# Optimization experiments

Hardware: AMD Instinct MI355X
Metric: run time of the kernel (lower is better)

## Reference

```python
import jax, jax.numpy as jnp
import numpy as np

DILS = [2 ** i for i in range(9)] * 7  # 27 residual-only layers + 36 layers with skip
N0 = 27  # first 27 layers (dilations0) do not contribute to skip connections


def _dconv(x, w, b, d):
    # dilated 'same' conv1d: x [B,C,T], w [O,I,3]
    y = jax.lax.conv_general_dilated(x, w, (1,), [(d, d)], rhs_dilation=(d,),
                                     dimension_numbers=('NCH', 'OIH', 'NCH'))
    return y + b[None, :, None]


def _pw(x, w, b):
    # 1x1 conv: w [O,C], x [B,C,T]
    return jnp.einsum('oc,bct->bot', w, x) + b[None, :, None]


def setup_inputs() -> dict:
    key = jax.random.key(0)
    ks = jax.random.split(key, 13)
    B, T, rd, sd, qd, L = 8, 16384, 128, 128, 256, 63
    s = 0.05
    f = lambda k, sh: jax.random.normal(k, sh, jnp.float32) * s
    return {
        'x': jax.random.normal(ks[0], (B, 1, T), jnp.float32),
        'causal_w': f(ks[1], (rd, 1, 25)),
        'causal_b': f(ks[2], (rd,)),
        'dcnn_w': f(ks[3], (L, rd, rd, 3)),
        'dcnn_b': f(ks[4], (L, rd)),
        'dense_w': f(ks[5], (L, rd, rd)),
        'dense_b': f(ks[6], (L, rd)),
        'skip_w': f(ks[7], (L, sd, rd)),
        'skip_b': f(ks[8], (L, sd)),
        'post1_w': f(ks[9], (sd, sd)),
        'post1_b': f(ks[10], (sd,)),
        'post2_w': f(ks[11], (qd, sd)),
        'post2_b': f(ks[12], (qd,)),
    }


def reference(x, causal_w, causal_b, dcnn_w, dcnn_b, dense_w, dense_b,
              skip_w, skip_b, post1_w, post1_b, post2_w, post2_b):
    # causal conv: kernel 25, padding 12 ('same')
    x = jax.lax.conv_general_dilated(x, causal_w, (1,), [(12, 12)],
                                     dimension_numbers=('NCH', 'OIH', 'NCH'))
    x = x + causal_b[None, :, None]
    B, _, T = x.shape
    skip = jnp.zeros((B, skip_w.shape[1], T), x.dtype)
    for cnt, d in enumerate(DILS):
        xin = x
        h = jax.nn.relu(x)
        h = jax.nn.relu(_dconv(h, dcnn_w[cnt], dcnn_b[cnt], d))
        if cnt >= N0:
            skip = skip + _pw(h, skip_w[cnt], skip_b[cnt])
        x = _pw(h, dense_w[cnt], dense_b[cnt]) + xin
    h = jax.nn.relu(_pw(jax.nn.relu(skip), post1_w, post1_b))
    return _pw(h, post2_w, post2_b)
```

## Files before the change

### kernel.cpp

```cpp
#include <hip/hip_runtime.h>

#define RD     128
#define TT     128
#define TLEN   16384
#define NB     8
#define NLAYER 63
#define N0SKIP 27
#define QD     256
#define PADR   136

typedef short bf16x8 __attribute__((ext_vector_type(8)));
typedef float f32x4  __attribute__((ext_vector_type(4)));

__device__ __forceinline__ unsigned short f2bf(float f) {
  unsigned u = __float_as_uint(f);
  u += 0x7fffu + ((u >> 16) & 1u);
  return (unsigned short)(u >> 16);
}
__device__ __forceinline__ short f2bf_relu(float f) {
  f = f > 0.f ? f : 0.f;
  unsigned u = __float_as_uint(f);
  u += 0x7fffu + ((u >> 16) & 1u);
  return (short)(u >> 16);
}

__device__ __forceinline__ void mfma_gemm(const unsigned short* __restrict__ aw,
                                          const short* sx, int rowbase,
                                          int c0w, int t0w, int n, int q,
                                          f32x4 (&acc)[4][4]) {
#pragma unroll
  for (int ks = 0; ks < 4; ++ks) {
    const int i0 = ks * 32 + q * 8;
    bf16x8 a[4], bb[4];
#pragma unroll
    for (int ct = 0; ct < 4; ++ct)
      a[ct] = *(const bf16x8*)&aw[(size_t)(c0w + ct * 16 + n) * RD + i0];
#pragma unroll
    for (int tt = 0; tt < 4; ++tt)
      bb[tt] = *(const bf16x8*)&sx[(rowbase + t0w + tt * 16 + n) * PADR + i0];
#pragma unroll
    for (int ct = 0; ct < 4; ++ct)
#pragma unroll
      for (int tt = 0; tt < 4; ++tt)
        acc[ct][tt] = __builtin_amdgcn_mfma_f32_16x16x32_bf16(a[ct], bb[tt],
                                                              acc[ct][tt], 0, 0, 0);
  }
}

__device__ __forceinline__ void zero_acc(f32x4 (&acc)[4][4]) {
#pragma unroll
  for (int i = 0; i < 4; ++i)
#pragma unroll
    for (int j = 0; j < 4; ++j) acc[i][j] = (f32x4){0.f, 0.f, 0.f, 0.f};
}

__device__ __forceinline__ void stage_rows(short* sx, int rowbase,
                                           const float* __restrict__ xb,
                                           int tstart, int nrows, int tid) {
  for (int idx = tid; idx < nrows * 32; idx += 256) {
    const int r = idx >> 5, c4 = (idx & 31) << 2;
    const int tg = tstart + r;
    float4 v = make_float4(0.f, 0.f, 0.f, 0.f);
    if ((unsigned)tg < (unsigned)TLEN)
      v = *(const float4*)&xb[(size_t)tg * RD + c4];
    short4 o;
    o.x = f2bf_relu(v.x); o.y = f2bf_relu(v.y);
    o.z = f2bf_relu(v.z); o.w = f2bf_relu(v.w);
    *(short4*)&sx[(rowbase + r) * PADR + c4] = o;
  }
}

__device__ __forceinline__ void store_act_bf16(short* dst, const f32x4 (&acc)[4][4],
                                               const float* __restrict__ bias,
                                               int c0w, int t0w, int n, int q) {
#pragma unroll
  for (int ct = 0; ct < 4; ++ct) {
    const int c = c0w + ct * 16 + q * 4;
    const float4 bb = *(const float4*)&bias[c];
#pragma unroll
    for (int tt = 0; tt < 4; ++tt) {
      const int t = t0w + tt * 16 + n;
      const f32x4 A = acc[ct][tt];
      short4 o;
      o.x = f2bf_relu(A[0] + bb.x);
      o.y = f2bf_relu(A[1] + bb.y);
      o.z = f2bf_relu(A[2] + bb.z);
      o.w = f2bf_relu(A[3] + bb.w);
      *(short4*)&dst[t * PADR + c] = o;
    }
  }
}

__device__ __forceinline__ void epi_accum(float* __restrict__ dst,
                                          const float* __restrict__ src,
                                          const float* __restrict__ bias,
                                          const f32x4 (&acc)[4][4],
                                          int c0w, int t0w, int n, int q) {
#pragma unroll
  for (int ct = 0; ct < 4; ++ct) {
    const int c = c0w + ct * 16 + q * 4;
    const float4 bb = *(const float4*)&bias[c];
#pragma unroll
    for (int tt = 0; tt < 4; ++tt) {
      const int t = t0w + tt * 16 + n;
      float4 r = *(const float4*)&src[(size_t)t * RD + c];
      const f32x4 A = acc[ct][tt];
      r.x += A[0] + bb.x; r.y += A[1] + bb.y;
      r.z += A[2] + bb.z; r.w += A[3] + bb.w;
      *(float4*)&dst[(size_t)t * RD + c] = r;
    }
  }
}

__global__ __launch_bounds__(256, 2) void layer_kernel(
    const float* __restrict__ x_in, float* __restrict__ x_out,
    float* __restrict__ skip,
    const unsigned short* __restrict__ wconv,
    const float* __restrict__ bconv,
    const unsigned short* __restrict__ wdense, const float* __restrict__ bdense,
    const unsigned short* __restrict__ wskip,  const float* __restrict__ bskip,
    int dil, int do_skip) {
  __shared__ short sx[256 * PADR];

  const int tid = threadIdx.x;
  const int b   = blockIdx.x >> 7;
  const int t0  = (blockIdx.x & 127) << 7;
  const int lane = tid & 63;
  const int n = lane & 15, q = lane >> 4;
  const int w = tid >> 6;
  const int c0w = (w & 1) * 64, t0w = (w >> 1) * 64;
  const float* xb = x_in + (size_t)b * TLEN * RD;

  f32x4 acc[4][4];
  zero_acc(acc);

  if (dil <= 64) {
    stage_rows(sx, 0, xb, t0 - dil, 128 + 2 * dil, tid);
    __syncthreads();
    for (int k = 0; k < 3; ++k)
      mfma_gemm(wconv + (size_t)k * RD * RD, sx, k * dil, c0w, t0w, n, q, acc);
  } else {
    stage_rows(sx, 0, xb, t0 - dil, 128, tid);
    __syncthreads();
    stage_rows(sx, 128, xb, t0, 128, tid);
    mfma_gemm(wconv, sx, 0, c0w, t0w, n, q, acc);
    __syncthreads();
    stage_rows(sx, 0, xb, t0 + dil, 128, tid);
    mfma_gemm(wconv + (size_t)RD * RD, sx, 128, c0w, t0w, n, q, acc);
    __syncthreads();
    mfma_gemm(wconv + (size_t)2 * RD * RD, sx, 0, c0w, t0w, n, q, acc);
  }
  __syncthreads();

  store_act_bf16(sx, acc, bconv, c0w, t0w, n, q);
  __syncthreads();

  zero_acc(acc);
  mfma_gemm(wdense, sx, 0, c0w, t0w, n, q, acc);
  {
    float* xo = x_out + ((size_t)b * TLEN + t0) * RD;
    const float* xi = x_in + ((size_t)b * TLEN + t0) * RD;
    epi_accum(xo, xi, bdense, acc, c0w, t0w, n, q);
  }

  if (do_skip) {
    zero_acc(acc);
    mfma_gemm(wskip, sx, 0, c0w, t0w, n, q, acc);
    float* sp = skip + ((size_t)b * TLEN + t0) * RD;
    epi_accum(sp, sp, bskip, acc, c0w, t0w, n, q);
  }
}

__global__ __launch_bounds__(256) void causal_kernel(const float* __restrict__ x,
                                                     const float* __restrict__ w,
                                                     const float* __restrict__ bias,
                                                     float* __restrict__ y) {
  __shared__ float xw[152];
  __shared__ float wl[RD * 25];
  __shared__ float bl[RD];
  const int tid = threadIdx.x;
  const int b   = blockIdx.x >> 7;
  const int t0  = (blockIdx.x & 127) << 7;
  for (int i = tid; i < RD * 25; i += 256) wl[i] = w[i];
  if (tid < RD) bl[tid] = bias[tid];
  for (int i = tid; i < 152; i += 256) {
    const int tg = t0 - 12 + i;
    xw[i] = ((unsigned)tg < (unsigned)TLEN) ? x[(size_t)b * TLEN + tg] : 0.f;
  }
  __syncthreads();
  const int c = tid & 127, tp = tid >> 7;
  float* yb = y + ((size_t)b * TLEN + t0) * RD + c;
  const float bc = bl[c];
  for (int i = 0; i < 64; ++i) {
    const int tl = i * 2 + tp;
    float s = bc;
#pragma unroll
    for (int k = 0; k < 25; ++k) s = fmaf(wl[c * 25 + k], xw[tl + k], s);
    yb[(size_t)tl * RD] = s;
  }
}

__global__ __launch_bounds__(256, 1) void post_kernel(
    const float* __restrict__ skip,
    const unsigned short* __restrict__ p1, const float* __restrict__ p1b,
    const unsigned short* __restrict__ p2, const float* __restrict__ p2b,
    float* __restrict__ out) {
  __shared__ short sb[128 * PADR];
  __shared__ short h1[128 * PADR];
  __shared__ float ost[128 * 132];

  const int tid = threadIdx.x;
  const int b   = blockIdx.x >> 7;
  const int t0  = (blockIdx.x & 127) << 7;
  const int lane = tid & 63;
  const int n = lane & 15, q = lane >> 4;
  const int w = tid >> 6;
  const int c0w = (w & 1) * 64, t0w = (w >> 1) * 64;
  const float* skb = skip + ((size_t)b * TLEN + t0) * RD;

  for (int idx = tid; idx < 128 * 32; idx += 256) {
    const int r = idx >> 5, c4 = (idx & 31) << 2;
    float4 v = *(const float4*)&skb[(size_t)r * RD + c4];
    short4 o;
    o.x = f2bf_relu(v.x); o.y = f2bf_relu(v.y);
    o.z = f2bf_relu(v.z); o.w = f2bf_relu(v.w);
    *(short4*)&sb[r * PADR + c4] = o;
  }
  __syncthreads();

  f32x4 acc[4][4];
  zero_acc(acc);
  mfma_gemm(p1, sb, 0, c0w, t0w, n, q, acc);
  store_act_bf16(h1, acc, p1b, c0w, t0w, n, q);
  __syncthreads();

  for (int half = 0; half < 2; ++half) {
    zero_acc(acc);
    mfma_gemm(p2 + (size_t)half * RD * RD, h1, 0, c0w, t0w, n, q, acc);
#pragma unroll
    for (int ct = 0; ct < 4; ++ct) {
      const int c = c0w + ct * 16 + q * 4;
      const float4 bb = *(const float4*)&p2b[half * RD + c];
#pragma unroll
      for (int tt = 0; tt < 4; ++tt) {
        const int t = t0w + tt * 16 + n;
        const f32x4 A = acc[ct][tt];
        ost[(c + 0) * 132 + t] = A[0] + bb.x;
        ost[(c + 1) * 132 + t] = A[1] + bb.y;
        ost[(c + 2) * 132 + t] = A[2] + bb.z;
        ost[(c + 3) * 132 + t] = A[3] + bb.w;
      }
    }
    __syncthreads();
    float* ob = out + ((size_t)b * QD + half * RD) * TLEN + t0;
    for (int idx = tid; idx < 128 * 32; idx += 256) {
      const int r = idx >> 5, t4 = (idx & 31) << 2;
      const float4 v = *(const float4*)&ost[r * 132 + t4];
      *(float4*)&ob[(size_t)r * TLEN + t4] = v;
    }
    __syncthreads();
  }
}

__global__ __launch_bounds__(256) void cvt_kernel(const float* __restrict__ in,
                                                  unsigned short* __restrict__ out,
                                                  int total) {
  const int i = blockIdx.x * 256 + threadIdx.x;
  if (i < total) out[i] = f2bf(in[i]);
}
__global__ __launch_bounds__(256) void cvt_conv_kernel(const float* __restrict__ in,
                                                       unsigned short* __restrict__ out,
                                                       int total) {
  const int idx = blockIdx.x * 256 + threadIdx.x;
  if (idx >= total) return;
  const int ci = idx & 127, co = (idx >> 7) & 127, lk = idx >> 14;
  const int k = lk % 3, l = lk / 3;
  out[idx] = f2bf(in[(((size_t)l * RD + co) * RD + ci) * 3 + k]);
}

extern "C" void kernel_launch(void* const* d_in, const int* in_sizes, int n_in,
                              void* d_out, int out_size, void* d_ws, size_t ws_size,
                              hipStream_t stream) {
  const float* x        = (const float*)d_in[0];
  const float* causal_w = (const float*)d_in[1];
  const float* causal_b = (const float*)d_in[2];
  const float* dcnn_w   = (const float*)d_in[3];
  const float* dcnn_b   = (const float*)d_in[4];
  const float* dense_w  = (const float*)d_in[5];
  const float* dense_b  = (const float*)d_in[6];
  const float* skip_w   = (const float*)d_in[7];
  const float* skip_b   = (const float*)d_in[8];
  const float* post1_w  = (const float*)d_in[9];
  const float* post1_b  = (const float*)d_in[10];
  const float* post2_w  = (const float*)d_in[11];
  const float* post2_b  = (const float*)d_in[12];
  float* out = (float*)d_out;

  const size_t XN = (size_t)NB * TLEN * RD;
  float* ws  = (float*)d_ws;
  float* xA  = ws;
  float* xB  = xA + XN;
  float* skp = xB + XN;
  unsigned short* wc  = (unsigned short*)(skp + XN);
  unsigned short* wd  = wc  + (size_t)NLAYER * 3 * RD * RD;
  unsigned short* wsk = wd  + (size_t)NLAYER * RD * RD;
  unsigned short* p1  = wsk + (size_t)NLAYER * RD * RD;
  unsigned short* p2  = p1  + RD * RD;

  const int tconv = NLAYER * 3 * RD * RD;
  const int t2    = NLAYER * RD * RD;
  cvt_conv_kernel<<<(tconv + 255) / 256, 256, 0, stream>>>(dcnn_w, wc, tconv);
  cvt_kernel<<<(t2 + 255) / 256, 256, 0, stream>>>(dense_w, wd, t2);
  cvt_kernel<<<(t2 + 255) / 256, 256, 0, stream>>>(skip_w, wsk, t2);
  cvt_kernel<<<(RD * RD + 255) / 256, 256, 0, stream>>>(post1_w, p1, RD * RD);
  cvt_kernel<<<(QD * RD + 255) / 256, 256, 0, stream>>>(post2_w, p2, QD * RD);

  causal_kernel<<<NB * (TLEN / TT), 256, 0, stream>>>(x, causal_w, causal_b, xA);
  hipMemsetAsync(skp, 0, XN * sizeof(float), stream);

  const float* src = xA;
  float* dst = xB;
  for (int l = 0; l < NLAYER; ++l) {
    const int dil = 1 << (l % 9);
    layer_kernel<<<NB * (TLEN / TT), 256, 0, stream>>>(
        src, dst, skp,
        wc  + (size_t)l * 3 * RD * RD, dcnn_b  + (size_t)l * RD,
        wd  + (size_t)l * RD * RD,     dense_b + (size_t)l * RD,
        wsk + (size_t)l * RD * RD,     skip_b  + (size_t)l * RD,
        dil, (l >= N0SKIP) ? 1 : 0);
    const float* tmp = src; src = dst; dst = (float*)tmp;
  }

  post_kernel<<<NB * (TLEN / TT), 256, 0, stream>>>(skp, p1, post1_b, p2, post2_b, out);
}
```

Measured before the change: 5.231 ms.

## Store bf16 relu'd activations, defer skip GEMMs into gather kernel with post-processing

Each layer now writes a bf16 copy of relu(x) next to the fp32 residual. The next layer stages bf16 directly into a 192-row circular shared buffer with no conversion, which raises occupancy to 3 blocks per SM. Per-layer skip accumulation (an fp32 read-modify-write of the skip tensor) is replaced by storing the bf16 hidden activations. A gather kernel then runs all skip GEMMs in one register accumulation with double-buffered staging, fused with the post1/post2 layers. This trades extra workspace (up to 36 bf16 activation copies) and extra bf16 writes for less fp32 skip traffic and one fewer kernel.

After: 7.559 ms. 44.5% more time.

```diff
diff --git a/kernel.cpp b/kernel.cpp
--- a/kernel.cpp
+++ b/kernel.cpp
@@ -6,8 +6,10 @@
 #define NB     8
 #define NLAYER 63
 #define N0SKIP 27
+#define NSKIP  36
 #define QD     256
 #define PADR   136
+#define CROWS  192
 
 typedef short bf16x8 __attribute__((ext_vector_type(8)));
 typedef float f32x4  __attribute__((ext_vector_type(4)));
@@ -24,9 +26,25 @@
   return (short)(u >> 16);
 }
 
+__device__ __forceinline__ void zero_acc(f32x4 (&acc)[4][4]) {
+#pragma unroll
+  for (int i = 0; i < 4; ++i)
+#pragma unroll
+    for (int j = 0; j < 4; ++j) acc[i][j] = (f32x4){0.f, 0.f, 0.f, 0.f};
+}
+
+__device__ __forceinline__ void mk_rows(int rows[4], int t0w, int n, int s) {
+#pragma unroll
+  for (int tt = 0; tt < 4; ++tt) {
+    int r = t0w + tt * 16 + n + s;
+    if (r >= CROWS) r -= CROWS;
+    rows[tt] = r;
+  }
+}
+
 __device__ __forceinline__ void mfma_gemm(const unsigned short* __restrict__ aw,
-                                          const short* sx, int rowbase,
-                                          int c0w, int t0w, int n, int q,
+                                          const short* sx, const int rows[4],
+                                          int c0w, int n, int q,
                                           f32x4 (&acc)[4][4]) {
 #pragma unroll
   for (int ks = 0; ks < 4; ++ks) {
@@ -37,7 +55,7 @@
       a[ct] = *(const bf16x8*)&aw[(size_t)(c0w + ct * 16 + n) * RD + i0];
 #pragma unroll
     for (int tt = 0; tt < 4; ++tt)
-      bb[tt] = *(const bf16x8*)&sx[(rowbase + t0w + tt * 16 + n) * PADR + i0];
+      bb[tt] = *(const bf16x8*)&sx[rows[tt] * PADR + i0];
 #pragma unroll
     for (int ct = 0; ct < 4; ++ct)
 #pragma unroll
@@ -47,26 +65,26 @@
   }
 }
 
-__device__ __forceinline__ void zero_acc(f32x4 (&acc)[4][4]) {
-#pragma unroll
-  for (int i = 0; i < 4; ++i)
-#pragma unroll
-    for (int j = 0; j < 4; ++j) acc[i][j] = (f32x4){0.f, 0.f, 0.f, 0.f};
-}
-
-__device__ __forceinline__ void stage_rows(short* sx, int rowbase,
-                                           const float* __restrict__ xb,
-                                           int tstart, int nrows, int tid) {
-  for (int idx = tid; idx < nrows * 32; idx += 256) {
-    const int r = idx >> 5, c4 = (idx & 31) << 2;
+__device__ __forceinline__ void stage_circ(short* sx, const unsigned short* __restrict__ xrb,
+                                           int tstart, int count, int slot0, int tid) {
+  const int tot = count << 4;
+  for (int idx = tid; idx < tot; idx += 256) {
+    const int r = idx >> 4, ck = (idx & 15) << 3;
     const int tg = tstart + r;
-    float4 v = make_float4(0.f, 0.f, 0.f, 0.f);
+    int4 v = {0, 0, 0, 0};
     if ((unsigned)tg < (unsigned)TLEN)
-      v = *(const float4*)&xb[(size_t)tg * RD + c4];
-    short4 o;
-    o.x = f2bf_relu(v.x); o.y = f2bf_relu(v.y);
-    o.z = f2bf_relu(v.z); o.w = f2bf_relu(v.w);
-    *(short4*)&sx[(rowbase + r) * PADR + c4] = o;
+      v = *(const int4*)&xrb[(size_t)tg * RD + ck];
+    int slot = slot0 + r;
+    if (slot >= CROWS) slot -= CROWS;
+    *(int4*)&sx[slot * PADR + ck] = v;
+  }
+}
+
+__device__ __forceinline__ void stage_tile(short* dst, const unsigned short* __restrict__ src,
+                                           int tid) {
+  for (int idx = tid; idx < 128 * 16; idx += 256) {
+    const int r = idx >> 4, ck = (idx & 15) << 3;
+    *(int4*)&dst[r * PADR + ck] = *(const int4*)&src[(size_t)r * RD + ck];
   }
 }
 
@@ -112,15 +130,16 @@
   }
 }
 
-__global__ __launch_bounds__(256, 2) void layer_kernel(
-    const float* __restrict__ x_in, float* __restrict__ x_out,
+__global__ __launch_bounds__(256, 3) void layer_kernel(
+    const unsigned short* __restrict__ xr_in, const float* __restrict__ x_in,
+    float* __restrict__ x_out, unsigned short* __restrict__ xr_out,
+    unsigned short* __restrict__ h_out,
     float* __restrict__ skip,
-    const unsigned short* __restrict__ wconv,
-    const float* __restrict__ bconv,
+    const unsigned short* __restrict__ wconv, const float* __restrict__ bconv,
     const unsigned short* __restrict__ wdense, const float* __restrict__ bdense,
-    const unsigned short* __restrict__ wskip,  const float* __restrict__ bskip,
-    int dil, int do_skip) {
-  __shared__ short sx[256 * PADR];
+    const unsigned short* __restrict__ wskip, const float* __restrict__ bskip,
+    int dil) {
+  __shared__ short sx[CROWS * PADR];
 
   const int tid = threadIdx.x;
   const int b   = blockIdx.x >> 7;
@@ -129,52 +148,196 @@
   const int n = lane & 15, q = lane >> 4;
   const int w = tid >> 6;
   const int c0w = (w & 1) * 64, t0w = (w >> 1) * 64;
-  const float* xb = x_in + (size_t)b * TLEN * RD;
+  const unsigned short* xrb = xr_in + (size_t)b * TLEN * RD;
 
   f32x4 acc[4][4];
   zero_acc(acc);
-
-  if (dil <= 64) {
-    stage_rows(sx, 0, xb, t0 - dil, 128 + 2 * dil, tid);
+  int rows[4];
+
+  if (dil <= 32) {
+    stage_circ(sx, xrb, t0 - dil, 128 + 2 * dil, 0, tid);
     __syncthreads();
-    for (int k = 0; k < 3; ++k)
-      mfma_gemm(wconv + (size_t)k * RD * RD, sx, k * dil, c0w, t0w, n, q, acc);
+#pragma unroll
+    for (int k = 0; k < 3; ++k) {
+      mk_rows(rows, t0w, n, k * dil);
+      mfma_gemm(wconv + (size_t)k * RD * RD, sx, rows, c0w, n, q, acc);
+    }
+  } else if (dil == 64) {
+    stage_circ(sx, xrb, t0 - 64, 192, 0, tid);
+    __syncthreads();
+    mk_rows(rows, t0w, n, 0);
+    mfma_gemm(wconv, sx, rows, c0w, n, q, acc);
+    mk_rows(rows, t0w, n, 64);
+    mfma_gemm(wconv + (size_t)RD * RD, sx, rows, c0w, n, q, acc);
+    __syncthreads();
+    stage_circ(sx, xrb, t0 + 128, 64, 0, tid);
+    __syncthreads();
+    mk_rows(rows, t0w, n, 128);
+    mfma_gemm(wconv + (size_t)2 * RD * RD, sx, rows, c0w, n, q, acc);
   } else {
-    stage_rows(sx, 0, xb, t0 - dil, 128, tid);
-    __syncthreads();
-    stage_rows(sx, 128, xb, t0, 128, tid);
-    mfma_gemm(wconv, sx, 0, c0w, t0w, n, q, acc);
-    __syncthreads();
-    stage_rows(sx, 0, xb, t0 + dil, 128, tid);
-    mfma_gemm(wconv + (size_t)RD * RD, sx, 128, c0w, t0w, n, q, acc);
-    __syncthreads();
-    mfma_gemm(wconv + (size_t)2 * RD * RD, sx, 0, c0w, t0w, n, q, acc);
+    for (int k = 0; k < 3; ++k) {
+      const int s = (k * dil) % CROWS;
+      stage_circ(sx, xrb, t0 + (k - 1) * dil, 128, s, tid);
+      __syncthreads();
+      mk_rows(rows, t0w, n, s);
+      mfma_gemm(wconv + (size_t)k * RD * RD, sx, rows, c0w, n, q, acc);
+      __syncthreads();
+    }
   }
   __syncthreads();
 
   store_act_bf16(sx, acc, bconv, c0w, t0w, n, q);
   __syncthreads();
 
+  if (h_out) {
+    unsigned short* hb = h_out + ((size_t)b * TLEN + t0) * RD;
+    for (int idx = tid; idx < 128 * 16; idx += 256) {
+      const int r = idx >> 4, ck = (idx & 15) << 3;
+      *(int4*)&hb[(size_t)r * RD + ck] = *(const int4*)&sx[r * PADR + ck];
+    }
+  }
+
   zero_acc(acc);
-  mfma_gemm(wdense, sx, 0, c0w, t0w, n, q, acc);
+  mk_rows(rows, t0w, n, 0);
+  mfma_gemm(wdense, sx, rows, c0w, n, q, acc);
   {
-    float* xo = x_out + ((size_t)b * TLEN + t0) * RD;
-    const float* xi = x_in + ((size_t)b * TLEN + t0) * RD;
-    epi_accum(xo, xi, bdense, acc, c0w, t0w, n, q);
-  }
-
-  if (do_skip) {
+    const size_t rowb = (size_t)b * TLEN + t0;
+    float* xo = x_out + rowb * RD;
+    const float* xi = x_in + rowb * RD;
+    unsigned short* xro = xr_out + rowb * RD;
+#pragma unroll
+    for (int ct = 0; ct < 4; ++ct) {
+      const int c = c0w + ct * 16 + q * 4;
+      const float4 bb = *(const float4*)&bdense[c];
+#pragma unroll
+      for (int tt = 0; tt < 4; ++tt) {
+        const int t = t0w + tt * 16 + n;
+        float4 r = *(const float4*)&xi[(size_t)t * RD + c];
+        const f32x4 A = acc[ct][tt];
+        r.x += A[0] + bb.x; r.y += A[1] + bb.y;
+        r.z += A[2] + bb.z; r.w += A[3] + bb.w;
+        *(float4*)&xo[(size_t)t * RD + c] = r;
+        short4 o;
+        o.x = f2bf_relu(r.x); o.y = f2bf_relu(r.y);
+        o.z = f2bf_relu(r.z); o.w = f2bf_relu(r.w);
+        *(short4*)&xro[(size_t)t * RD + c] = o;
+      }
+    }
+  }
+
+  if (skip) {
     zero_acc(acc);
-    mfma_gemm(wskip, sx, 0, c0w, t0w, n, q, acc);
+    mfma_gemm(wskip, sx, rows, c0w, n, q, acc);
     float* sp = skip + ((size_t)b * TLEN + t0) * RD;
     epi_accum(sp, sp, bskip, acc, c0w, t0w, n, q);
+  }
+}
+
+__global__ __launch_bounds__(256, 2) void gather_kernel(
+    const unsigned short* __restrict__ h, int nl,
+    const unsigned short* __restrict__ wsk_g,
+    float* __restrict__ skip_io, int skip_rd, int skip_wr, int do_final,
+    const float* __restrict__ bsum,
+    const unsigned short* __restrict__ p1, const float* __restrict__ p1b,
+    const unsigned short* __restrict__ p2, const float* __restrict__ p2b,
+    float* __restrict__ out) {
+  __shared__ short buf[2][128 * PADR];
+
+  const int tid = threadIdx.x;
+  const int b   = blockIdx.x >> 7;
+  const int t0  = (blockIdx.x & 127) << 7;
+  const int lane = tid & 63;
+  const int n = lane & 15, q = lane >> 4;
+  const int w = tid >> 6;
+  const int c0w = (w & 1) * 64, t0w = (w >> 1) * 64;
+  const size_t tilebase = ((size_t)b * TLEN + t0) * RD;
+  const size_t XNE = (size_t)NB * TLEN * RD;
+
+  f32x4 acc[4][4];
+  zero_acc(acc);
+  int rows[4];
+  mk_rows(rows, t0w, n, 0);
+
+  if (nl > 0) {
+    stage_tile(buf[0], h + tilebase, tid);
+    __syncthreads();
+    for (int li = 0; li < nl; ++li) {
+      const int cur = li & 1;
+      if (li + 1 < nl)
+        stage_tile(buf[cur ^ 1], h + (size_t)(li + 1) * XNE + tilebase, tid);
+      mfma_gemm(wsk_g + (size_t)li * RD * RD, buf[cur], rows, c0w, n, q, acc);
+      __syncthreads();
+    }
+  }
+
+  if (!do_final) {
+    float* sp = skip_io + tilebase;
+#pragma unroll
+    for (int ct = 0; ct < 4; ++ct) {
+      const int c = c0w + ct * 16 + q * 4;
+#pragma unroll
+      for (int tt = 0; tt < 4; ++tt) {
+        const int t = t0w + tt * 16 + n;
+        const f32x4 A = acc[ct][tt];
+        float4 r = make_float4(A[0], A[1], A[2], A[3]);
+        if (skip_rd) {
+          const float4 s = *(const float4*)&sp[(size_t)t * RD + c];
+          r.x += s.x; r.y += s.y; r.z += s.z; r.w += s.w;
+        }
+        *(float4*)&sp[(size_t)t * RD + c] = r;
+      }
+    }
+    return;
+  }
+
+  if (skip_rd) {
+    const float* sp = skip_io + tilebase;
+#pragma unroll
+    for (int ct = 0; ct < 4; ++ct) {
+      const int c = c0w + ct * 16 + q * 4;
+#pragma unroll
+      for (int tt = 0; tt < 4; ++tt) {
+        const int t = t0w + tt * 16 + n;
+        const float4 s = *(const float4*)&sp[(size_t)t * RD + c];
+        acc[ct][tt][0] += s.x; acc[ct][tt][1] += s.y;
+        acc[ct][tt][2] += s.z; acc[ct][tt][3] += s.w;
+      }
+    }
+  }
+
+  store_act_bf16(buf[0], acc, bsum, c0w, t0w, n, q);
+  __syncthreads();
+  zero_acc(acc);
+  mfma_gemm(p1, buf[0], rows, c0w, n, q, acc);
+  store_act_bf16(buf[1], acc, p1b, c0w, t0w, n, q);
+  __syncthreads();
+
+  for (int half = 0; half < 2; ++half) {
+    zero_acc(acc);
+    mfma_gemm(p2 + (size_t)half * RD * RD, buf[1], rows, c0w, n, q, acc);
+    const size_t ob = ((size_t)b * QD + half * RD) * TLEN + t0;
+#pragma unroll
+    for (int ct = 0; ct < 4; ++ct) {
+      const int c = c0w + ct * 16 + q * 4;
+      const float4 bb = *(const float4*)&p2b[half * RD + c];
+#pragma unroll
+      for (int tt = 0; tt < 4; ++tt) {
+        const int t = t0w + tt * 16 + n;
+        const f32x4 A = acc[ct][tt];
+        out[ob + (size_t)(c + 0) * TLEN + t] = A[0] + bb.x;
+        out[ob + (size_t)(c + 1) * TLEN + t] = A[1] + bb.y;
+        out[ob + (size_t)(c + 2) * TLEN + t] = A[2] + bb.z;
+        out[ob + (size_t)(c + 3) * TLEN + t] = A[3] + bb.w;
+      }
+    }
   }
 }
 
 __global__ __launch_bounds__(256) void causal_kernel(const float* __restrict__ x,
                                                      const float* __restrict__ w,
                                                      const float* __restrict__ bias,
-                                                     float* __restrict__ y) {
+                                                     float* __restrict__ y,
+                                                     unsigned short* __restrict__ yr) {
   __shared__ float xw[152];
   __shared__ float wl[RD * 25];
   __shared__ float bl[RD];
@@ -190,6 +353,7 @@
   __syncthreads();
   const int c = tid & 127, tp = tid >> 7;
   float* yb = y + ((size_t)b * TLEN + t0) * RD + c;
+  unsigned short* yrb = yr + ((size_t)b * TLEN + t0) * RD + c;
   const float bc = bl[c];
   for (int i = 0; i < 64; ++i) {
     const int tl = i * 2 + tp;
@@ -197,68 +361,7 @@
 #pragma unroll
     for (int k = 0; k < 25; ++k) s = fmaf(wl[c * 25 + k], xw[tl + k], s);
     yb[(size_t)tl * RD] = s;
-  }
-}
-
-__global__ __launch_bounds__(256, 1) void post_kernel(
-    const float* __restrict__ skip,
-    const unsigned short* __restrict__ p1, const float* __restrict__ p1b,
-    const unsigned short* __restrict__ p2, const float* __restrict__ p2b,
-    float* __restrict__ out) {
-  __shared__ short sb[128 * PADR];
-  __shared__ short h1[128 * PADR];
-  __shared__ float ost[128 * 132];
-
-  const int tid = threadIdx.x;
-  const int b   = blockIdx.x >> 7;
-  const int t0  = (blockIdx.x & 127) << 7;
-  const int lane = tid & 63;
-  const int n = lane & 15, q = lane >> 4;
-  const int w = tid >> 6;
-  const int c0w = (w & 1) * 64, t0w = (w >> 1) * 64;
-  const float* skb = skip + ((size_t)b * TLEN + t0) * RD;
-
-  for (int idx = tid; idx < 128 * 32; idx += 256) {
-    const int r = idx >> 5, c4 = (idx & 31) << 2;
-    float4 v = *(const float4*)&skb[(size_t)r * RD + c4];
-    short4 o;
-    o.x = f2bf_relu(v.x); o.y = f2bf_relu(v.y);
-    o.z = f2bf_relu(v.z); o.w = f2bf_relu(v.w);
-    *(short4*)&sb[r * PADR + c4] = o;
-  }
-  __syncthreads();
-
-  f32x4 acc[4][4];
-  zero_acc(acc);
-  mfma_gemm(p1, sb, 0, c0w, t0w, n, q, acc);
-  store_act_bf16(h1, acc, p1b, c0w, t0w, n, q);
-  __syncthreads();
-
-  for (int half = 0; half < 2; ++half) {
-    zero_acc(acc);
-    mfma_gemm(p2 + (size_t)half * RD * RD, h1, 0, c0w, t0w, n, q, acc);
-#pragma unroll
-    for (int ct = 0; ct < 4; ++ct) {
-      const int c = c0w + ct * 16 + q * 4;
-      const float4 bb = *(const float4*)&p2b[half * RD + c];
-#pragma unroll
-      for (int tt = 0; tt < 4; ++tt) {
-        const int t = t0w + tt * 16 + n;
-        const f32x4 A = acc[ct][tt];
-        ost[(c + 0) * 132 + t] = A[0] + bb.x;
-        ost[(c + 1) * 132 + t] = A[1] + bb.y;
-        ost[(c + 2) * 132 + t] = A[2] + bb.z;
-        ost[(c + 3) * 132 + t] = A[3] + bb.w;
-      }
-    }
-    __syncthreads();
-    float* ob = out + ((size_t)b * QD + half * RD) * TLEN + t0;
-    for (int idx = tid; idx < 128 * 32; idx += 256) {
-      const int r = idx >> 5, t4 = (idx & 31) << 2;
-      const float4 v = *(const float4*)&ost[r * 132 + t4];
-      *(float4*)&ob[(size_t)r * TLEN + t4] = v;
-    }
-    __syncthreads();
+    yrb[(size_t)tl * RD] = (unsigned short)f2bf_relu(s);
   }
 }
 
@@ -276,6 +379,12 @@
   const int ci = idx & 127, co = (idx >> 7) & 127, lk = idx >> 14;
   const int k = lk % 3, l = lk / 3;
   out[idx] = f2bf(in[(((size_t)l * RD + co) * RD + ci) * 3 + k]);
+}
+__global__ void bsum_kernel(const float* __restrict__ sb, float* __restrict__ bsum) {
+  const int c = threadIdx.x;
+  float s = 0.f;
+  for (int l = N0SKIP; l < NLAYER; ++l) s += sb[l * RD + c];
+  bsum[c] = s;
 }
 
 extern "C" void kernel_launch(void* const* d_in, const int* in_sizes, int n_in,
@@ -296,16 +405,37 @@
   const float* post2_b  = (const float*)d_in[12];
   float* out = (float*)d_out;
 
-  const size_t XN = (size_t)NB * TLEN * RD;
-  float* ws  = (float*)d_ws;
-  float* xA  = ws;
-  float* xB  = xA + XN;
-  float* skp = xB + XN;
-  unsigned short* wc  = (unsigned short*)(skp + XN);
-  unsigned short* wd  = wc  + (size_t)NLAYER * 3 * RD * RD;
-  unsigned short* wsk = wd  + (size_t)NLAYER * RD * RD;
-  unsigned short* p1  = wsk + (size_t)NLAYER * RD * RD;
-  unsigned short* p2  = p1  + RD * RD;
+  const size_t XNE = (size_t)NB * TLEN * RD;
+
+  char* p = (char*)d_ws;
+  float* xA  = (float*)p;            p += XNE * 4;
+  float* xB  = (float*)p;            p += XNE * 4;
+  float* bsm = (float*)p;            p += 512;
+  unsigned short* wc  = (unsigned short*)p; p += (size_t)NLAYER * 3 * RD * RD * 2;
+  unsigned short* wd  = (unsigned short*)p; p += (size_t)NLAYER * RD * RD * 2;
+  unsigned short* wsk = (unsigned short*)p; p += (size_t)NLAYER * RD * RD * 2;
+  unsigned short* p1  = (unsigned short*)p; p += RD * RD * 2;
+  unsigned short* p2  = (unsigned short*)p; p += QD * RD * 2;
+  unsigned short* xrA = (unsigned short*)p; p += XNE * 2;
+  unsigned short* xrB = (unsigned short*)p; p += XNE * 2;
+  const size_t base_used = (size_t)(p - (char*)d_ws);
+
+  const size_t need_full = base_used + (size_t)NSKIP * XNE * 2;
+  const size_t need_g9   = base_used + XNE * 4 + (size_t)9 * XNE * 2;
+  const size_t need_fb   = base_used + XNE * 4;
+  int G;
+  if (ws_size >= need_full)      G = NSKIP;
+  else if (ws_size >= need_g9)   G = 9;
+  else                           G = 0;
+
+  float* skp = nullptr;
+  unsigned short* hb = nullptr;
+  if (G == NSKIP) {
+    hb = (unsigned short*)p;
+  } else {
+    skp = (float*)p; p += XNE * 4;
+    if (G == 9) hb = (unsigned short*)p;
+  }
 
   const int tconv = NLAYER * 3 * RD * RD;
   const int t2    = NLAYER * RD * RD;
@@ -314,22 +444,50 @@
   cvt_kernel<<<(t2 + 255) / 256, 256, 0, stream>>>(skip_w, wsk, t2);
   cvt_kernel<<<(RD * RD + 255) / 256, 256, 0, stream>>>(post1_w, p1, RD * RD);
   cvt_kernel<<<(QD * RD + 255) / 256, 256, 0, stream>>>(post2_w, p2, QD * RD);
-
-  causal_kernel<<<NB * (TLEN / TT), 256, 0, stream>>>(x, causal_w, causal_b, xA);
-  hipMemsetAsync(skp, 0, XN * sizeof(float), stream);
-
-  const float* src = xA;
-  float* dst = xB;
+  if (G > 0) bsum_kernel<<<1, RD, 0, stream>>>(skip_b, bsm);
+  else       hipMemsetAsync(bsm, 0, 512, stream);
+  if (G == 0) hipMemsetAsync(skp, 0, XNE * 4, stream);
+
+  causal_kernel<<<NB * (TLEN / TT), 256, 0, stream>>>(x, causal_w, causal_b, xA, xrA);
+
+  const int grid = NB * (TLEN / TT);
+  const float* xs = xA;  float* xd = xB;
+  const unsigned short* xrs = xrA;  unsigned short* xrd = xrB;
+
   for (int l = 0; l < NLAYER; ++l) {
     const int dil = 1 << (l % 9);
-    layer_kernel<<<NB * (TLEN / TT), 256, 0, stream>>>(
-        src, dst, skp,
+    unsigned short* hout = nullptr;
+    float* skarg = nullptr;
+    if (l >= N0SKIP) {
+      if (G > 0) hout = hb + (size_t)((l - N0SKIP) % G) * XNE;
+      else       skarg = skp;
+    }
+    layer_kernel<<<grid, 256, 0, stream>>>(
+        xrs, xs, xd, xrd, hout, skarg,
         wc  + (size_t)l * 3 * RD * RD, dcnn_b  + (size_t)l * RD,
         wd  + (size_t)l * RD * RD,     dense_b + (size_t)l * RD,
         wsk + (size_t)l * RD * RD,     skip_b  + (size_t)l * RD,
-        dil, (l >= N0SKIP) ? 1 : 0);
-    const float* tmp = src; src = dst; dst = (float*)tmp;
-  }
-
-  post_kernel<<<NB * (TLEN / TT), 256, 0, stream>>>(skp, p1, post1_b, p2, post2_b, out);
-}
+        dil);
+    { const float* t = xs; xs = xd; xd = (float*)t; }
+    { const unsigned short* t = xrs; xrs = xrd; xrd = (unsigned short*)t; }
+
+    if (G == 9 && l >= N0SKIP && ((l - N0SKIP) % 9) == 8) {
+      const int g = (l - N0SKIP) / 9;
+      const int l0 = N0SKIP + g * 9;
+      const int final_g = (g == 3);
+      gather_kernel<<<grid, 256, 0, stream>>>(
+          hb, 9, wsk + (size_t)l0 * RD * RD,
+          skp, (g > 0) ? 1 : 0, final_g ? 0 : 1, final_g,
+          bsm, p1, post1_b, p2, post2_b, out);
+    }
+  }
+
+  if (G == NSKIP) {
+    gather_kernel<<<grid, 256, 0, stream>>>(
+        hb, NSKIP, wsk + (size_t)N0SKIP * RD * RD,
+        nullptr, 0, 0, 1, bsm, p1, post1_b, p2, post2_b, out);
+  } else if (G == 0) {
+    gather_kernel<<<grid, 256, 0, stream>>>(
+        nullptr, 0, nullptr, skp, 1, 0, 1, bsm, p1, post1_b, p2, post2_b, out);
+  }
+}
```
